# Performance work log

Hardware: AMD Instinct MI355X
Metric: run time of the kernel (lower is better)

The kernel has to match this reference:

```python
import jax, jax.numpy as jnp
import numpy as np

N = 8192      # nodes
E = 262144    # edges (avg degree 32)
D = 128       # embed dim
F = 128       # input feature dim
H = 128       # GCN hidden
C = 7         # classes
EPS = 1e-4    # sample_bias for concrete noise


def setup_inputs() -> dict:
    key = jax.random.key(0)
    ks = jax.random.split(key, 10)
    x = jax.random.normal(ks[0], (N, F), jnp.float32)
    embed = jax.random.normal(ks[1], (N, D), jnp.float32)
    row = jax.random.randint(ks[2], (E,), 0, N, jnp.int64)
    col = jax.random.randint(ks[3], (E,), 0, N, jnp.int64)
    adj_data = jnp.ones((E,), jnp.float32)
    # uniform noise in (bias, 1-bias) as in concrete_sample(training=True)
    noise = jax.random.uniform(ks[4], (E,), jnp.float32, EPS, 1.0 - EPS)
    tmp = jnp.ones((1,), jnp.float32)  # temperature beta
    W1e = jax.random.normal(ks[5], (3 * D, 64), jnp.float32) * 0.05
    b1e = jnp.zeros((64,), jnp.float32)
    W2e = jax.random.normal(ks[6], (64, 1), jnp.float32) * 0.05
    b2e = jnp.zeros((1,), jnp.float32)
    Wg0 = jax.random.normal(ks[7], (F, H), jnp.float32) * 0.05
    Wg1 = jax.random.normal(ks[8], (H, C), jnp.float32) * 0.05
    return {"x": x, "embed": embed, "adj_data": adj_data, "noise": noise,
            "tmp": tmp, "W1e": W1e, "b1e": b1e, "W2e": W2e, "b2e": b2e,
            "Wg0": Wg0, "Wg1": Wg1, "row": row, "col": col, "nodeid": 5}


def reference(x, embed, adj_data, noise, tmp, W1e, b1e, W2e, b2e, Wg0, Wg1,
              row, col, nodeid):
    # gather node embeddings per edge + self node embedding, concat -> [E, 3D]
    f1 = embed[row]
    f2 = embed[col]
    selfemb = jnp.broadcast_to(embed[nodeid][None, :], (f1.shape[0], D))
    f12self = jnp.concatenate([f1, f2, selfemb], axis=-1)
    # 2-layer explainer MLP -> per-edge logit
    h = jax.nn.relu(f12self @ W1e + b1e)
    log_alpha = (h @ W2e + b2e).reshape(-1)  # [E]
    # concrete-sigmoid reparameterization (training=True path, noise supplied)
    gate_inputs = (jnp.log(noise) - jnp.log1p(-noise) + log_alpha) / tmp[0]
    values = jax.nn.sigmoid(gate_inputs)
    # scatter edge gates and adjacency values into dense [N, N]
    mask = jnp.zeros((N, N), jnp.float32).at[row, col].add(values)
    adj = jnp.zeros((N, N), jnp.float32).at[row, col].add(adj_data)
    # symmetrize mask, apply to adjacency, zero the diagonal
    sym_mask = (mask + mask.T) * 0.5
    masked_adj = adj * sym_mask * (1.0 - jnp.eye(N, dtype=jnp.float32))
    # wrapped GNN: 2-layer GCN
    h1 = jax.nn.relu(masked_adj @ (x @ Wg0))
    out = masked_adj @ (h1 @ Wg1)
    node_pred = out[nodeid]  # [C]
    return jax.nn.softmax(node_pred, axis=0)
```

## Files before the change

### kernel.cpp

```cpp
#include <hip/hip_runtime.h>
#include <hip/hip_bf16.h>
#include <math.h>

#define NNODES 8192
#define DIM 128
#define SMAX 128
#define HSIZE 16384
#define LDA2 68

__device__ __forceinline__ int detect64(const void* rowp) {
    const long long* p = (const long long*)rowp;
    int is64 = 1;
#pragma unroll
    for (int i = 0; i < 4; i++) {
        long long v = p[i];
        if (v < 0 || v >= NNODES) is64 = 0;
    }
    return is64;
}

__device__ __forceinline__ int edge_idx(const void* p, int e, int idx64) {
    if (idx64) return (int)((const long long*)p)[e];
    return ((const int*)p)[e];
}

__device__ __forceinline__ int hash_insert(unsigned int* hashK, unsigned int key1) {
    unsigned int h = (key1 * 2654435761u) & (HSIZE - 1);
    for (;;) {
        unsigned int prev = atomicCAS(&hashK[h], 0u, key1);
        if (prev == 0u || prev == key1) return (int)h;
        h = (h + 1) & (HSIZE - 1);
    }
}


__global__ __launch_bounds__(256) void k_zero(float4* z, int n4) {
    int i = blockIdx.x * blockDim.x + threadIdx.x;
    if (i < n4) z[i] = make_float4(0.f, 0.f, 0.f, 0.f);
}

__global__ __launch_bounds__(256) void k_dense(
        const float* embed, const float* W1e, const float* b1e,
        const int* nodep, const void* rowp, const void* colp, const float* adjd,
        float* U, float* V, float* cself,
        int* flags, float* cnt0, int* nbr, int* slotmap,
        float* hzero, int nhz, int E) {
    int bid = blockIdx.x;
    int t = threadIdx.x;
    int gid = bid * 256 + t;
    int nodeid = nodep[0];
    int tile = bid >> 1;
    int colh = bid & 1;

    __shared__ float At[128 * LDA2];
    __shared__ float Wl[128 * LDA2];
    __shared__ float semb[DIM];

    for (int i = gid; i < nhz; i += 256 * 256) hzero[i] = 0.f;

    const float* Asrc = embed + (size_t)tile * 64 * DIM;
    for (int i = t; i < 64 * DIM; i += 256)
        At[(i & 127) * LDA2 + (i >> 7)] = Asrc[i];
    int doff = colh * 128;
    for (int i = t; i < 128 * 64; i += 256)
        Wl[(i >> 6) * LDA2 + (i & 63)] = W1e[(size_t)(doff + (i >> 6)) * 64 + (i & 63)];
    if (bid == 0 && t < DIM) semb[t] = embed[(size_t)nodeid * DIM + t];
    __syncthreads();

    int rg = t & 15;
    int cg = t >> 4;
    float acc[4][4];
#pragma unroll
    for (int i = 0; i < 4; i++)
#pragma unroll
        for (int j = 0; j < 4; j++) acc[i][j] = 0.f;

#pragma unroll 4
    for (int d = 0; d < DIM; d++) {
        float4 a4 = *(const float4*)&At[d * LDA2 + rg * 4];
        float4 w4 = *(const float4*)&Wl[d * LDA2 + cg * 4];
        const float* ap = &a4.x;
        const float* wp = &w4.x;
#pragma unroll
        for (int i = 0; i < 4; i++)
#pragma unroll
            for (int j = 0; j < 4; j++)
                acc[i][j] = fmaf(ap[i], wp[j], acc[i][j]);
    }

    float* o = colh ? V : U;
    int n0 = tile * 64;
#pragma unroll
    for (int i = 0; i < 4; i++)
        *(float4*)&o[(size_t)(n0 + rg * 4 + i) * 64 + cg * 4] =
            make_float4(acc[i][0], acc[i][1], acc[i][2], acc[i][3]);

    if (bid == 0 && t < 64) {
        float a = b1e[t];
        for (int d = 0; d < DIM; d++)
            a += semb[d] * W1e[(size_t)(2 * DIM + d) * 64 + t];
        cself[t] = a;
    }

    int idx64 = detect64(rowp);
    for (int e = gid; e < E; e += 256 * 256) {
        int r = edge_idx(rowp, e, idx64);
        if (r != nodeid) continue;
        int c = edge_idx(colp, e, idx64);
        if (c == nodeid) continue;
        atomicAdd(&cnt0[c], adjd[e]);
        if (atomicCAS((unsigned int*)&slotmap[c], 0u, 0xFFFFFFFFu) == 0u) {
            int s = atomicAdd(&flags[1], 1);
            if (s < SMAX) {
                nbr[s] = c;
                __hip_atomic_store(&slotmap[c], s + 1, __ATOMIC_RELAXED,
                                   __HIP_MEMORY_SCOPE_AGENT);
            }
        }
    }
}

__global__ __launch_bounds__(1024) void k_gates(
        const float* adjd, const float* noise, const float* tmp,
        const float* W2e, const float* b2e,
        const void* rowp, const void* colp, const int* nodep,
        const float* U, const float* V, const float* cself,
        const int* slotmap,
        unsigned int* hashK, float* hashC, float* hashF, float* hashR,
        float* f0s, float* r0s, int E) {
    __shared__ int lq[1024];
    __shared__ int lqn;
    int t = threadIdx.x;
    if (t == 0) lqn = 0;
    __syncthreads();
    int idx64 = detect64(rowp);
    int nodeid = nodep[0];
    int e = blockIdx.x * 1024 + t;
    if (e < E) {
        int r = edge_idx(rowp, e, idx64);
        int c = edge_idx(colp, e, idx64);
        if (r != c) {
            int spr = slotmap[r];
            int spc = slotmap[c];
            if (spr > 0 || spc > 0) lq[atomicAdd(&lqn, 1)] = e;
        }
    }
    __syncthreads();
    int n = lqn;
    for (int i = t; i < n; i += 1024) {
        int e2 = lq[i];
        int r = edge_idx(rowp, e2, idx64);
        int c = edge_idx(colp, e2, idx64);
        int spr = slotmap[r];
        int spc = slotmap[c];
        float la = b2e[0];
        const float4* u4 = (const float4*)(U + (size_t)r * 64);
        const float4* v4 = (const float4*)(V + (size_t)c * 64);
        const float4* c4 = (const float4*)cself;
        const float4* w4 = (const float4*)W2e;
#pragma unroll
        for (int d = 0; d < 16; d++) {
            float4 uu = u4[d], vv = v4[d], cc = c4[d], ww = w4[d];
            float h0 = uu.x + vv.x + cc.x;
            float h1 = uu.y + vv.y + cc.y;
            float h2 = uu.z + vv.z + cc.z;
            float h3 = uu.w + vv.w + cc.w;
            la += (h0 > 0.f ? h0 : 0.f) * ww.x + (h1 > 0.f ? h1 : 0.f) * ww.y
                + (h2 > 0.f ? h2 : 0.f) * ww.z + (h3 > 0.f ? h3 : 0.f) * ww.w;
        }
        float nz = noise[e2];
        float gi = (logf(nz) - log1pf(-nz) + la) / tmp[0];
        float v = 1.f / (1.f + expf(-gi));
        if (spr > 0) {
            int sr = spr - 1;
            unsigned int key1 = ((unsigned int)(sr << 13) | (unsigned int)c) + 1u;
            int idx = hash_insert(hashK, key1);
            atomicAdd(&hashC[idx], adjd[e2]);
            atomicAdd(&hashF[idx], v);
            if (c == nodeid) atomicAdd(&r0s[sr], v);
        }
        if (spc > 0) {
            int sc = spc - 1;
            unsigned int key1 = ((unsigned int)(sc << 13) | (unsigned int)r) + 1u;
            int idx = hash_insert(hashK, key1);
            atomicAdd(&hashR[idx], v);
            if (r == nodeid) atomicAdd(&f0s[sc], v);
        }
    }
}

__global__ __launch_bounds__(1024) void k_hagg(
        const unsigned int* hashK, const float* hashC, const float* hashF,
        const float* hashR, const float* x, float* xagg) {
    int gid = blockIdx.x * blockDim.x + threadIdx.x;
    int group = gid >> 7;
    int tg = gid & 127;
    int ngroups = (256 * 1024) >> 7;
    for (int entry = group; entry < HSIZE; entry += ngroups) {
        unsigned int key1 = hashK[entry];
        if (key1 == 0u) continue;
        float wgt = hashC[entry] * (hashF[entry] + hashR[entry]) * 0.5f;
        if (wgt == 0.f) continue;
        unsigned int key = key1 - 1u;
        int s = (int)(key >> 13);
        int k = (int)(key & 8191u);
        atomicAdd(&xagg[(size_t)s * DIM + tg], wgt * x[(size_t)k * DIM + tg]);
    }
}

__global__ __launch_bounds__(128) void k_final(
        const int* flags, const float* xagg, const float* cnt0, const int* nbr,
        const float* f0s, const float* r0s, const float* Wg0, const float* Wg1,
        float* glogits, int* done, float* out) {
    int b = blockIdx.x, t = threadIdx.x;
    int ns = flags[1]; if (ns > SMAX) ns = SMAX;
    if (b < ns) {
        __shared__ float xs[DIM];
        __shared__ float pacc[2][7];
        xs[t] = xagg[(size_t)b * DIM + t];
        __syncthreads();
        float h = 0.f;
        for (int d = 0; d < DIM; d++) h = fmaf(xs[d], Wg0[d * DIM + t], h);
        h = h > 0.f ? h : 0.f;
        int wave = t >> 6, lane = t & 63;
        float part[7];
        for (int c = 0; c < 7; c++) {
            float p = h * Wg1[t * 7 + c];
            for (int o = 32; o >= 1; o >>= 1) p += __shfl_xor(p, o, 64);
            part[c] = p;
        }
        if (lane == 0)
            for (int c = 0; c < 7; c++) pacc[wave][c] = part[c];
        __syncthreads();
        if (t == 0) {
            float a0 = cnt0[nbr[b]] * (f0s[b] + r0s[b]) * 0.5f;
            for (int c = 0; c < 7; c++)
                atomicAdd(&glogits[c * 16], a0 * (pacc[0][c] + pacc[1][c]));
        }
    }
    if (t != 0) return;
    asm volatile("s_waitcnt vmcnt(0)" ::: "memory");
    int old = __hip_atomic_fetch_add(done, 1, __ATOMIC_RELAXED,
                                     __HIP_MEMORY_SCOPE_AGENT);
    if (old != SMAX - 1) return;
    float v[7], m = -1e30f, ssum = 0.f;
    for (int c = 0; c < 7; c++) {
        v[c] = __hip_atomic_load(&glogits[c * 16], __ATOMIC_RELAXED,
                                 __HIP_MEMORY_SCOPE_AGENT);
        if (v[c] > m) m = v[c];
    }
    for (int c = 0; c < 7; c++) { v[c] = expf(v[c] - m); ssum += v[c]; }
    for (int c = 0; c < 7; c++) out[c] = v[c] / ssum;
}

extern "C" void kernel_launch(void* const* d_in, const int* in_sizes, int n_in,
                              void* d_out, int out_size, void* d_ws, size_t ws_size,
                              hipStream_t stream) {
    const float* x     = (const float*)d_in[0];
    const float* embed = (const float*)d_in[1];
    const float* adjd  = (const float*)d_in[2];
    const float* noise = (const float*)d_in[3];
    const float* tmp   = (const float*)d_in[4];
    const float* W1e   = (const float*)d_in[5];
    const float* b1e   = (const float*)d_in[6];
    const float* W2e   = (const float*)d_in[7];
    const float* b2e   = (const float*)d_in[8];
    const float* Wg0   = (const float*)d_in[9];
    const float* Wg1   = (const float*)d_in[10];
    const void*  rowp  = d_in[11];
    const void*  colp  = d_in[12];
    const int*   nodep = (const int*)d_in[13];
    int E = in_sizes[3];

    char* w = (char*)d_ws;
    size_t off = 0;
    auto alloc = [&](size_t bytes) -> char* {
        char* p = w + off;
        off = (off + bytes + 255) & ~(size_t)255;
        return p;
    };
    float*        cself   = (float*)alloc(64 * 4);
    int*          nbr     = (int*)  alloc(SMAX * 4);
    float*        U       = (float*)alloc((size_t)NNODES * 64 * 4);
    float*        V       = (float*)alloc((size_t)NNODES * 64 * 4);
    char*         zstart  = w + off;
    int*          flags   = (int*)  alloc(256);
    float*        glogits = (float*)alloc(512);
    int*          slotmap = (int*)  alloc((size_t)NNODES * 4);
    float*        cnt0    = (float*)alloc((size_t)NNODES * 4);
    float*        f0s     = (float*)alloc(SMAX * 4);
    float*        r0s     = (float*)alloc(SMAX * 4);
    size_t zbytes  = (size_t)((w + off) - zstart);
    unsigned int* hashK   = (unsigned int*)alloc((size_t)HSIZE * 4);
    float*        hashC   = (float*)alloc((size_t)HSIZE * 4);
    float*        hashF   = (float*)alloc((size_t)HSIZE * 4);
    float*        hashR   = (float*)alloc((size_t)HSIZE * 4);
    float*        xagg    = (float*)alloc((size_t)SMAX * DIM * 4);
    int nhz = HSIZE * 4 + SMAX * DIM;
    int n4 = (int)(zbytes / 16);

    k_zero<<<(n4 + 255) / 256, 256, 0, stream>>>((float4*)zstart, n4);
    k_dense<<<256, 256, 0, stream>>>(embed, W1e, b1e, nodep, rowp, colp, adjd,
                                     U, V, cself, flags, cnt0, nbr, slotmap,
                                     (float*)hashK, nhz, E);
    k_gates<<<(E + 1023) / 1024, 1024, 0, stream>>>(adjd, noise, tmp, W2e, b2e,
                                           rowp, colp, nodep, U, V, cself,
                                           slotmap, hashK, hashC, hashF, hashR,
                                           f0s, r0s, E);
    k_hagg<<<256, 1024, 0, stream>>>(hashK, hashC, hashF, hashR, x, xagg);
    k_final<<<SMAX, 128, 0, stream>>>(flags, xagg, cnt0, nbr, f0s, r0s,
                                      Wg0, Wg1, glogits, &flags[2],
                                      (float*)d_out);
}
```

Before: 43.62 us.

## Fuse hash aggregation and final GCN stage into one kernel with grid barrier

Merges the hash-table aggregation kernel and the final per-slot GCN/softmax kernel into a single launch of 128 blocks. An atomic counter spin-wait acts as a grid-wide barrier between the two phases, so one kernel launch and its inter-kernel gap go away. The aggregation phase now runs on half as many threads, and the design depends on all blocks being co-resident and on the new counter being zeroed beforehand.

```diff
diff --git a/kernel.cpp b/kernel.cpp
--- a/kernel.cpp
+++ b/kernel.cpp
@@ -7,6 +7,7 @@
 #define SMAX 128
 #define HSIZE 16384
 #define LDA2 68
+#define NBT 128
 
 __device__ __forceinline__ int detect64(const void* rowp) {
     const long long* p = (const long long*)rowp;
@@ -189,14 +190,17 @@
     }
 }
 
-__global__ __launch_bounds__(1024) void k_hagg(
-        const unsigned int* hashK, const float* hashC, const float* hashF,
-        const float* hashR, const float* x, float* xagg) {
-    int gid = blockIdx.x * blockDim.x + threadIdx.x;
+__global__ __launch_bounds__(1024) void k_tail(
+        const int* flags, const unsigned int* hashK, const float* hashC,
+        const float* hashF, const float* hashR, const float* x,
+        const float* cnt0, const int* nbr, const float* f0s, const float* r0s,
+        const float* Wg0, const float* Wg1,
+        float* xagg, float* glogits, int* arr, int* done, float* out) {
+    int bid = blockIdx.x, t = threadIdx.x;
+    int gid = bid * 1024 + t;
     int group = gid >> 7;
-    int tg = gid & 127;
-    int ngroups = (256 * 1024) >> 7;
-    for (int entry = group; entry < HSIZE; entry += ngroups) {
+    int tg = t & 127;
+    for (int entry = group; entry < HSIZE; entry += NBT * 8) {
         unsigned int key1 = hashK[entry];
         if (key1 == 0u) continue;
         float wgt = hashC[entry] * (hashF[entry] + hashR[entry]) * 0.5f;
@@ -206,34 +210,41 @@
         int k = (int)(key & 8191u);
         atomicAdd(&xagg[(size_t)s * DIM + tg], wgt * x[(size_t)k * DIM + tg]);
     }
-}
-
-__global__ __launch_bounds__(128) void k_final(
-        const int* flags, const float* xagg, const float* cnt0, const int* nbr,
-        const float* f0s, const float* r0s, const float* Wg0, const float* Wg1,
-        float* glogits, int* done, float* out) {
-    int b = blockIdx.x, t = threadIdx.x;
+    __syncthreads();
+    if (t == 0) {
+        asm volatile("s_waitcnt vmcnt(0)" ::: "memory");
+        __hip_atomic_fetch_add(arr, 1, __ATOMIC_RELAXED,
+                               __HIP_MEMORY_SCOPE_AGENT);
+        while (__hip_atomic_load(arr, __ATOMIC_RELAXED,
+                                 __HIP_MEMORY_SCOPE_AGENT) < NBT)
+            __builtin_amdgcn_s_sleep(2);
+        __builtin_amdgcn_fence(__ATOMIC_ACQUIRE, "agent");
+    }
+    __syncthreads();
+
     int ns = flags[1]; if (ns > SMAX) ns = SMAX;
-    if (b < ns) {
+    if (bid < ns) {
         __shared__ float xs[DIM];
         __shared__ float pacc[2][7];
-        xs[t] = xagg[(size_t)b * DIM + t];
+        if (t < DIM) xs[t] = xagg[(size_t)bid * DIM + t];
         __syncthreads();
-        float h = 0.f;
-        for (int d = 0; d < DIM; d++) h = fmaf(xs[d], Wg0[d * DIM + t], h);
-        h = h > 0.f ? h : 0.f;
-        int wave = t >> 6, lane = t & 63;
-        float part[7];
-        for (int c = 0; c < 7; c++) {
-            float p = h * Wg1[t * 7 + c];
-            for (int o = 32; o >= 1; o >>= 1) p += __shfl_xor(p, o, 64);
-            part[c] = p;
-        }
-        if (lane == 0)
-            for (int c = 0; c < 7; c++) pacc[wave][c] = part[c];
+        if (t < DIM) {
+            float h = 0.f;
+            for (int d = 0; d < DIM; d++) h = fmaf(xs[d], Wg0[d * DIM + t], h);
+            h = h > 0.f ? h : 0.f;
+            int wave = t >> 6, lane = t & 63;
+            float part[7];
+            for (int c = 0; c < 7; c++) {
+                float p = h * Wg1[t * 7 + c];
+                for (int o = 32; o >= 1; o >>= 1) p += __shfl_xor(p, o, 64);
+                part[c] = p;
+            }
+            if (lane == 0)
+                for (int c = 0; c < 7; c++) pacc[wave][c] = part[c];
+        }
         __syncthreads();
         if (t == 0) {
-            float a0 = cnt0[nbr[b]] * (f0s[b] + r0s[b]) * 0.5f;
+            float a0 = cnt0[nbr[bid]] * (f0s[bid] + r0s[bid]) * 0.5f;
             for (int c = 0; c < 7; c++)
                 atomicAdd(&glogits[c * 16], a0 * (pacc[0][c] + pacc[1][c]));
         }
@@ -242,7 +253,7 @@
     asm volatile("s_waitcnt vmcnt(0)" ::: "memory");
     int old = __hip_atomic_fetch_add(done, 1, __ATOMIC_RELAXED,
                                      __HIP_MEMORY_SCOPE_AGENT);
-    if (old != SMAX - 1) return;
+    if (old != NBT - 1) return;
     float v[7], m = -1e30f, ssum = 0.f;
     for (int c = 0; c < 7; c++) {
         v[c] = __hip_atomic_load(&glogits[c * 16], __ATOMIC_RELAXED,
@@ -307,8 +318,8 @@
                                            rowp, colp, nodep, U, V, cself,
                                            slotmap, hashK, hashC, hashF, hashR,
                                            f0s, r0s, E);
-    k_hagg<<<256, 1024, 0, stream>>>(hashK, hashC, hashF, hashR, x, xagg);
-    k_final<<<SMAX, 128, 0, stream>>>(flags, xagg, cnt0, nbr, f0s, r0s,
-                                      Wg0, Wg1, glogits, &flags[2],
-                                      (float*)d_out);
-}
+    k_tail<<<NBT, 1024, 0, stream>>>(flags, hashK, hashC, hashF, hashR, x,
+                                     cnt0, nbr, f0s, r0s, Wg0, Wg1,
+                                     xagg, glogits, &flags[2], &flags[3],
+                                     (float*)d_out);
+}
```

Result: slower. 50.56 us (+15.9%).
